# Kernel tuning notes

Hardware: AMD Instinct MI355X
Metric: run time of the kernel (lower is better)

## Reference

```python
import jax, jax.numpy as jnp
import numpy as np

IN, EMB, RNN, OUT = 2, 64, 128, 2
SEQ, PEDS, PRED = 20, 16384, 30


def setup_inputs() -> dict:
    key = jax.random.key(0)
    ks = jax.random.split(key, 6)
    def w(k, shape, fan_in):
        bound = 1.0 / np.sqrt(fan_in)
        return jax.random.uniform(k, shape, jnp.float32, -bound, bound)
    return {
        "observed_batch": jax.random.normal(ks[0], (SEQ, PEDS, IN), jnp.float32),
        "W_emb": w(ks[1], (EMB, IN), IN),
        "b_emb": jnp.zeros((EMB,), jnp.float32),
        "W_ih": w(ks[2], (4 * RNN, EMB), RNN),
        "b_ih": jnp.zeros((4 * RNN,), jnp.float32),
        "W_hh": w(ks[3], (4 * RNN, RNN), RNN),
        "b_hh": jnp.zeros((4 * RNN,), jnp.float32),
        "W_out": w(ks[4], (OUT, RNN), RNN),
        "b_out": jnp.zeros((OUT,), jnp.float32),
        "pred_len": PRED,
    }


def _lstm_cell(x, h, c, W_ih, b_ih, W_hh, b_hh):
    # torch.nn.LSTMCell gate order: i, f, g, o
    gates = x @ W_ih.T + b_ih + h @ W_hh.T + b_hh  # [peds, 4*RNN]
    i, f, g, o = jnp.split(gates, 4, axis=-1)
    i = jax.nn.sigmoid(i)
    f = jax.nn.sigmoid(f)
    g = jnp.tanh(g)
    o = jax.nn.sigmoid(o)
    c_new = f * c + i * g
    h_new = o * jnp.tanh(c_new)
    return h_new, c_new


def reference(observed_batch, W_emb, b_emb, W_ih, b_ih, W_hh, b_hh, W_out, b_out, pred_len):
    peds = observed_batch.shape[1]
    h0 = jnp.zeros((peds, RNN), observed_batch.dtype)
    c0 = jnp.zeros((peds, RNN), observed_batch.dtype)

    # Encode observed steps (dropout is identity in eval mode).
    def enc_step(carry, x_t):
        h, c = carry
        e = jax.nn.relu(x_t @ W_emb.T + b_emb)
        h, c = _lstm_cell(e, h, c, W_ih, b_ih, W_hh, b_hh)
        return (h, c), None

    (h, c), _ = jax.lax.scan(enc_step, (h0, c0), observed_batch)
    # Only the last step's output_layer result is consumed (faithful to source).
    out = h @ W_out.T + b_out  # [peds, OUT]

    def dec_step(carry, _):
        h, c, out = carry
        e = jax.nn.relu(out @ W_emb.T + b_emb)
        h, c = _lstm_cell(e, h, c, W_ih, b_ih, W_hh, b_hh)
        out = h @ W_out.T + b_out
        return (h, c, out), out

    _, output_seq = jax.lax.scan(dec_step, (h, c, out), None, length=pred_len)
    return jnp.squeeze(output_seq)  # [pred_len, peds, 2] (squeeze is a no-op here)
```

## Files before the change

### kernel.cpp

```cpp
#include <hip/hip_runtime.h>
#include <hip/hip_bf16.h>

#define SEQ   20
#define PRED  30
#define TSTEPS (SEQ + PRED)
#define PEDS  16384
#define EMB   64
#define RNN   128
#define PB    64
#define NT    512
#define L2E   1.44269504f

typedef _Float16 half8 __attribute__((ext_vector_type(8)));
typedef __attribute__((ext_vector_type(4))) float f32x4;
typedef __attribute__((ext_vector_type(2))) float f32x2;

#define RAW_BAR() do {                                          \
    asm volatile("s_waitcnt lgkmcnt(0)" ::: "memory");          \
    __builtin_amdgcn_s_barrier();                               \
    asm volatile("" ::: "memory");                              \
    __builtin_amdgcn_sched_barrier(0);                          \
} while (0)

__device__ __forceinline__ float sigm2(float xp) {
    return __builtin_amdgcn_rcpf(1.f + __builtin_amdgcn_exp2f(-xp));
}
__device__ __forceinline__ float tanh2p(float xp) {
    float r = __builtin_amdgcn_rcpf(__builtin_amdgcn_exp2f(xp + xp) + 1.f);
    return fmaf(-2.f, r, 1.f);
}
__device__ __forceinline__ float tanh2u(float x) {
    float r = __builtin_amdgcn_rcpf(__builtin_amdgcn_exp2f(x * (2.f * L2E)) + 1.f);
    return fmaf(-2.f, r, 1.f);
}

__global__ void prep_kernel(const float* __restrict__ Wih, const float* __restrict__ Whh,
                            const float* __restrict__ Wemb, const float* __restrict__ bemb,
                            _Float16* __restrict__ Bp, float* __restrict__ ewp) {
    int t = blockIdx.x * blockDim.x + threadIdx.x;
    if (t < 64) {
        ewp[t * 4 + 0] = Wemb[t * 2 + 0];
        ewp[t * 4 + 1] = Wemb[t * 2 + 1];
        ewp[t * 4 + 2] = bemb[t];
        ewp[t * 4 + 3] = 0.f;
    }
    if (t >= 6 * 32 * 64 * 8) return;
    int i  = t & 7;
    int l  = (t >> 3) & 63;
    int nt = (t >> 9) & 31;
    int kt = t >> 14;
    int n = (nt >> 3) * RNN + (nt & 7) * 16 + (l & 15);
    int k = kt * 32 + ((l >> 4) << 3) + i;
    float val = (k < EMB) ? Wih[n * EMB + k] : Whh[n * RNN + (k - EMB)];
    Bp[t] = (_Float16)(val * L2E);
}

__global__ __launch_bounds__(NT, 2) void lstm_kernel(
    const float* __restrict__ obs,
    const float* __restrict__ ewp,
    const float* __restrict__ bih,  const float* __restrict__ bhh,
    const _Float16* __restrict__ Bp,
    const float* __restrict__ Wout, const float* __restrict__ bout,
    float* __restrict__ out)
{
    __shared__ __align__(16) char smA[2 * 24576];
    __shared__ __align__(16) char smB[3 * 32768];
    __shared__ float smObs[SEQ * 128];
    __shared__ float smEW[64 * 4];
    __shared__ float smWO[256];
    __shared__ float part[64 * 2 * 4];
    __shared__ float outs[64 * 2];

    const int tid = threadIdx.x;
    const int l   = tid & 63;
    const int w   = __builtin_amdgcn_readfirstlane(tid >> 6);

    for (int r = tid; r < (2 * 24576) / 4; r += NT) ((int*)smA)[r] = 0;
    if (tid < 64) *(f32x4*)(smEW + tid * 4) = *(const f32x4*)(ewp + tid * 4);
    if (tid < 256) smWO[tid] = Wout[tid];
    for (int i = tid; i < SEQ * 128; i += NT) {
        int st = i >> 7, r = i & 127;
        smObs[i] = obs[(size_t)st * (PEDS * 2) + blockIdx.x * 128 + r];
    }

    const int jlane = w * 16 + (l & 15);
    const int lrow  = (l >> 4) << 2;
    const int swz   = (l & 7) << 4;

    float bias[4];
#pragma unroll
    for (int g = 0; g < 4; ++g) {
        int n = g * RNN + jlane;
        bias[g] = (bih[n] + bhh[n]) * L2E;
    }

    int aBase[4];
#pragma unroll
    for (int mt = 0; mt < 4; ++mt) {
        int ped = mt * 16 + (l & 15);
        aBase[mt] = ped * 384 + ((l >> 4) << 4);
    }
    int sAddr[4];
#pragma unroll
    for (int r = 0; r < 4; ++r) {
        int ped = lrow + r;
        sAddr[r] = (ped * 384 + 128 + jlane * 2) ^ ((ped & 7) << 4);
    }
    const int eAddr = (l * 384 + w * 16) ^ swz;
    const int oBase = l * 384 + 128 + (w >> 1) * 64;
    const char* bb  = smB + l * 16;
    const char* stageSrc = (const char*)Bp + l * 16 + w * 1024;
    const float* woBase = smWO + (w & 1) * 128 + (w >> 1) * 32;

    auto stage = [&](int slice) {
        const int buf = slice % 3;
#pragma unroll
        for (int g = 0; g < 4; ++g) {
            const void* src = stageSrc + slice * 32768 + g * 8192;
            __builtin_amdgcn_global_load_lds(
                (const __attribute__((address_space(1))) void*)src,
                (__attribute__((address_space(3))) void*)(smB + buf * 32768 + (g * 8 + w) * 1024),
                16, 0, 0);
        }
    };

    float c[16];
#pragma unroll
    for (int q = 0; q < 16; ++q) c[q] = 0.f;

    stage(0);
    stage(1);
    __syncthreads();

    int curOff = 0;

    for (int step = 0; step < TSTEPS; ++step) {
        const int nxtOff = curOff ^ 24576;

        {
            float x0, x1;
            if (step < SEQ) {
                f32x2 xv = *(const f32x2*)(smObs + step * 128 + l * 2);
                x0 = xv[0]; x1 = xv[1];
            } else {
                x0 = outs[l * 2 + 0];
                x1 = outs[l * 2 + 1];
            }
            half8 vh;
#pragma unroll
            for (int q = 0; q < 8; ++q) {
                const f32x4 ew = *(const f32x4*)(smEW + (w * 8 + q) * 4);
                float v = fmaf(x0, ew[0], fmaf(x1, ew[1], ew[2]));
                vh[q] = (_Float16)fmaxf(v, 0.f);
            }
            *(half8*)(smA + curOff + eAddr) = vh;
        }
        RAW_BAR();

        f32x4 acc[4][4];
#pragma unroll
        for (int mt = 0; mt < 4; ++mt)
#pragma unroll
            for (int g = 0; g < 4; ++g) {
                acc[mt][g][0] = bias[g]; acc[mt][g][1] = bias[g];
                acc[mt][g][2] = bias[g]; acc[mt][g][3] = bias[g];
            }
#pragma unroll
        for (int kt = 0; kt < 6; ++kt) {
            const int buf = kt % 3;
            stage((kt < 4) ? kt + 2 : kt - 4);
            asm volatile("s_waitcnt vmcnt(8)" ::: "memory");
            half8 bf[4];
#pragma unroll
            for (int g = 0; g < 4; ++g)
                bf[g] = *(const half8*)(bb + buf * 32768 + (g * 8 + w) * 1024);
#pragma unroll
            for (int mt = 0; mt < 4; ++mt) {
                half8 ah = *(const half8*)(smA + curOff + ((aBase[mt] + kt * 64) ^ swz));
#pragma unroll
                for (int g = 0; g < 4; ++g)
                    acc[mt][g] = __builtin_amdgcn_mfma_f32_16x16x32_f16(ah, bf[g], acc[mt][g], 0, 0, 0);
            }
        }

#pragma unroll
        for (int mt = 0; mt < 4; ++mt) {
#pragma unroll
            for (int r = 0; r < 4; ++r) {
                float gi = acc[mt][0][r], gf = acc[mt][1][r];
                float gg = acc[mt][2][r], go = acc[mt][3][r];
                float i_ = sigm2(gi), f_ = sigm2(gf), g_ = tanh2p(gg), o_ = sigm2(go);
                float cn = fmaf(f_, c[mt * 4 + r], i_ * g_);
                c[mt * 4 + r] = cn;
                float hn = o_ * tanh2u(cn);
                *(_Float16*)(smA + nxtOff + sAddr[r] + mt * 6144) = (_Float16)hn;
            }
        }

        if (step >= SEQ - 1) {
            RAW_BAR();
            {
                const int oo = w & 1;
                float s = 0.f;
#pragma unroll
                for (int t = 0; t < 4; ++t) {
                    half8 hh8 = *(const half8*)(smA + nxtOff + ((oBase + t * 16) ^ swz));
                    const f32x4 w0 = *(const f32x4*)(woBase + t * 8);
                    const f32x4 w1 = *(const f32x4*)(woBase + t * 8 + 4);
#pragma unroll
                    for (int i = 0; i < 4; ++i) {
                        s = fmaf((float)hh8[i], w0[i], s);
                        s = fmaf((float)hh8[i + 4], w1[i], s);
                    }
                }
                part[(l * 2 + oo) * 4 + (w >> 1)] = s;
            }
            RAW_BAR();
            if (tid < 128) {
                int pp = tid & 63, o2 = tid >> 6;
                const float* pr = &part[(pp * 2 + o2) * 4];
                float o = bout[o2] + ((pr[0] + pr[1]) + (pr[2] + pr[3]));
                outs[pp * 2 + o2] = o;
                if (step >= SEQ)
                    out[((size_t)(step - SEQ) * PEDS + blockIdx.x * PB + pp) * 2 + o2] = o;
            }
            RAW_BAR();
        }
        curOff = nxtOff;
    }
}

extern "C" void kernel_launch(void* const* d_in, const int* in_sizes, int n_in,
                              void* d_out, int out_size, void* d_ws, size_t ws_size,
                              hipStream_t stream) {
    const float* obs  = (const float*)d_in[0];
    const float* Wemb = (const float*)d_in[1];
    const float* bemb = (const float*)d_in[2];
    const float* Wih  = (const float*)d_in[3];
    const float* bih  = (const float*)d_in[4];
    const float* Whh  = (const float*)d_in[5];
    const float* bhh  = (const float*)d_in[6];
    const float* Wout = (const float*)d_in[7];
    const float* bout = (const float*)d_in[8];

    _Float16* Bp  = (_Float16*)d_ws;
    float*    ewp = (float*)(Bp + 6 * 32 * 64 * 8);

    prep_kernel<<<(6 * 32 * 64 * 8 + 255) / 256, 256, 0, stream>>>(Wih, Whh, Wemb, bemb, Bp, ewp);
    lstm_kernel<<<PEDS / PB, NT, 0, stream>>>(obs, ewp, bih, bhh, Bp, Wout, bout, (float*)d_out);
}
```

Baseline: 228.1 us.

## Fold output projection into decoder embedding via MFMA and double-buffer weight staging

Decoder steps no longer compute the output layer with scalar dot products, cross-wave partial sums and three barriers. Instead the prep kernel folds W_out into W_emb and b_emb, so the next embedding and the output come straight from h through a small fp16 MFMA over a 16x80 weight tile kept in LDS. The output is written one step late, with a final epilogue for the last step. Weight staging drops from triple to double buffering to make LDS room for the folded matrix, which may expose load latency, and fp16 rounding of the folded weights changes numerics slightly.

```diff
diff --git a/kernel.cpp b/kernel.cpp
--- a/kernel.cpp
+++ b/kernel.cpp
@@ -36,13 +36,25 @@
 
 __global__ void prep_kernel(const float* __restrict__ Wih, const float* __restrict__ Whh,
                             const float* __restrict__ Wemb, const float* __restrict__ bemb,
-                            _Float16* __restrict__ Bp, float* __restrict__ ewp) {
+                            const float* __restrict__ Wout, const float* __restrict__ bout,
+                            _Float16* __restrict__ Bp, float* __restrict__ ewp,
+                            _Float16* __restrict__ Xp, float* __restrict__ bfold) {
     int t = blockIdx.x * blockDim.x + threadIdx.x;
     if (t < 64) {
         ewp[t * 4 + 0] = Wemb[t * 2 + 0];
         ewp[t * 4 + 1] = Wemb[t * 2 + 1];
         ewp[t * 4 + 2] = bemb[t];
         ewp[t * 4 + 3] = 0.f;
+        bfold[t] = bemb[t] + Wemb[t * 2 + 0] * bout[0] + Wemb[t * 2 + 1] * bout[1];
+    }
+    if (t < 5 * 4 * 64 * 8) {
+        int i = t & 7, l = (t >> 3) & 63, ktp = (t >> 9) & 3, tile = t >> 11;
+        int c = tile * 16 + (l & 15);
+        int k = ktp * 32 + ((l >> 4) << 3) + i;
+        float v;
+        if (c < 64) v = Wemb[c * 2 + 0] * Wout[k] + Wemb[c * 2 + 1] * Wout[RNN + k];
+        else { int o = c - 64; v = (o < 2) ? Wout[o * RNN + k] : 0.f; }
+        Xp[t] = (_Float16)v;
     }
     if (t >= 6 * 32 * 64 * 8) return;
     int i  = t & 7;
@@ -59,25 +71,23 @@
     const float* __restrict__ obs,
     const float* __restrict__ ewp,
     const float* __restrict__ bih,  const float* __restrict__ bhh,
-    const _Float16* __restrict__ Bp,
-    const float* __restrict__ Wout, const float* __restrict__ bout,
+    const _Float16* __restrict__ Bp, const _Float16* __restrict__ Xp,
+    const float* __restrict__ bfold_g, const float* __restrict__ bout,
     float* __restrict__ out)
 {
     __shared__ __align__(16) char smA[2 * 24576];
-    __shared__ __align__(16) char smB[3 * 32768];
+    __shared__ __align__(16) char smB[2 * 32768];
+    __shared__ __align__(16) char smX[20480];
     __shared__ float smObs[SEQ * 128];
     __shared__ float smEW[64 * 4];
-    __shared__ float smWO[256];
-    __shared__ float part[64 * 2 * 4];
-    __shared__ float outs[64 * 2];
 
     const int tid = threadIdx.x;
     const int l   = tid & 63;
     const int w   = __builtin_amdgcn_readfirstlane(tid >> 6);
 
     for (int r = tid; r < (2 * 24576) / 4; r += NT) ((int*)smA)[r] = 0;
+    for (int r = tid; r < 20480 / 4; r += NT) ((int*)smX)[r] = ((const int*)Xp)[r];
     if (tid < 64) *(f32x4*)(smEW + tid * 4) = *(const f32x4*)(ewp + tid * 4);
-    if (tid < 256) smWO[tid] = Wout[tid];
     for (int i = tid; i < SEQ * 128; i += NT) {
         int st = i >> 7, r = i & 127;
         smObs[i] = obs[(size_t)st * (PEDS * 2) + blockIdx.x * 128 + r];
@@ -94,12 +104,25 @@
         bias[g] = (bih[n] + bhh[n]) * L2E;
     }
 
+    const int nU = (w < 4) ? 3 : 2;
+    int uT[3], uM[3];
+#pragma unroll
+    for (int j = 0; j < 3; ++j) { int u = w + j * 8; uT[j] = u % 5; uM[j] = u / 5; }
+    const float bo2 = ((l & 15) < 2) ? bout[l & 15] : 0.f;
+    float bx[3];
+    int axA[3], xAd[3], exCol2[3];
+    const int aB0 = (l & 15) * 384 + ((l >> 4) << 4);
+#pragma unroll
+    for (int j = 0; j < 3; ++j) {
+        bx[j]     = (uT[j] < 4) ? bfold_g[uT[j] * 16 + (l & 15)] : bo2;
+        axA[j]    = aB0 + uM[j] * 6144;
+        xAd[j]    = uT[j] * 4096 + l * 16;
+        exCol2[j] = (uT[j] * 16 + (l & 15)) * 2;
+    }
+
     int aBase[4];
 #pragma unroll
-    for (int mt = 0; mt < 4; ++mt) {
-        int ped = mt * 16 + (l & 15);
-        aBase[mt] = ped * 384 + ((l >> 4) << 4);
-    }
+    for (int mt = 0; mt < 4; ++mt) aBase[mt] = aB0 + mt * 6144;
     int sAddr[4];
 #pragma unroll
     for (int r = 0; r < 4; ++r) {
@@ -107,16 +130,13 @@
         sAddr[r] = (ped * 384 + 128 + jlane * 2) ^ ((ped & 7) << 4);
     }
     const int eAddr = (l * 384 + w * 16) ^ swz;
-    const int oBase = l * 384 + 128 + (w >> 1) * 64;
     const char* bb  = smB + l * 16;
     const char* stageSrc = (const char*)Bp + l * 16 + w * 1024;
-    const float* woBase = smWO + (w & 1) * 128 + (w >> 1) * 32;
-
-    auto stage = [&](int slice) {
-        const int buf = slice % 3;
+
+    auto stage = [&](int kt, int buf) {
 #pragma unroll
         for (int g = 0; g < 4; ++g) {
-            const void* src = stageSrc + slice * 32768 + g * 8192;
+            const void* src = stageSrc + kt * 32768 + g * 8192;
             __builtin_amdgcn_global_load_lds(
                 (const __attribute__((address_space(1))) void*)src,
                 (__attribute__((address_space(3))) void*)(smB + buf * 32768 + (g * 8 + w) * 1024),
@@ -128,8 +148,7 @@
 #pragma unroll
     for (int q = 0; q < 16; ++q) c[q] = 0.f;
 
-    stage(0);
-    stage(1);
+    stage(0, 0);
     __syncthreads();
 
     int curOff = 0;
@@ -137,25 +156,56 @@
     for (int step = 0; step < TSTEPS; ++step) {
         const int nxtOff = curOff ^ 24576;
 
-        {
-            float x0, x1;
-            if (step < SEQ) {
-                f32x2 xv = *(const f32x2*)(smObs + step * 128 + l * 2);
-                x0 = xv[0]; x1 = xv[1];
-            } else {
-                x0 = outs[l * 2 + 0];
-                x1 = outs[l * 2 + 1];
-            }
+        if (step < SEQ) {
+            f32x2 xv = *(const f32x2*)(smObs + step * 128 + l * 2);
             half8 vh;
 #pragma unroll
             for (int q = 0; q < 8; ++q) {
                 const f32x4 ew = *(const f32x4*)(smEW + (w * 8 + q) * 4);
-                float v = fmaf(x0, ew[0], fmaf(x1, ew[1], ew[2]));
+                float v = fmaf(xv[0], ew[0], fmaf(xv[1], ew[1], ew[2]));
                 vh[q] = (_Float16)fmaxf(v, 0.f);
             }
             *(half8*)(smA + curOff + eAddr) = vh;
-        }
-        RAW_BAR();
+            RAW_BAR();
+        } else {
+            RAW_BAR();
+            f32x4 ax[3];
+#pragma unroll
+            for (int j = 0; j < 3; ++j) {
+                ax[j][0] = bx[j]; ax[j][1] = bx[j]; ax[j][2] = bx[j]; ax[j][3] = bx[j];
+            }
+#pragma unroll
+            for (int ktp = 0; ktp < 4; ++ktp) {
+#pragma unroll
+                for (int j = 0; j < 3; ++j) {
+                    if (j < nU) {
+                        half8 ah = *(const half8*)(smA + curOff + ((axA[j] + (ktp + 2) * 64) ^ swz));
+                        half8 xb = *(const half8*)(smX + xAd[j] + ktp * 1024);
+                        ax[j] = __builtin_amdgcn_mfma_f32_16x16x32_f16(ah, xb, ax[j], 0, 0, 0);
+                    }
+                }
+            }
+#pragma unroll
+            for (int j = 0; j < 3; ++j) {
+                if (j < nU) {
+                    if (uT[j] < 4) {
+#pragma unroll
+                        for (int r = 0; r < 4; ++r) {
+                            int ped = uM[j] * 16 + lrow + r;
+                            int off = (ped * 384 + exCol2[j]) ^ ((ped & 7) << 4);
+                            *(_Float16*)(smA + curOff + off) = (_Float16)fmaxf(ax[j][r], 0.f);
+                        }
+                    } else if ((l & 15) < 2 && step > SEQ) {
+#pragma unroll
+                        for (int r = 0; r < 4; ++r) {
+                            int ped = uM[j] * 16 + lrow + r;
+                            out[((size_t)(step - 1 - SEQ) * PEDS + blockIdx.x * PB + ped) * 2 + (l & 15)] = ax[j][r];
+                        }
+                    }
+                }
+            }
+            RAW_BAR();
+        }
 
         f32x4 acc[4][4];
 #pragma unroll
@@ -167,9 +217,10 @@
             }
 #pragma unroll
         for (int kt = 0; kt < 6; ++kt) {
-            const int buf = kt % 3;
-            stage((kt < 4) ? kt + 2 : kt - 4);
-            asm volatile("s_waitcnt vmcnt(8)" ::: "memory");
+            const int buf = kt & 1;
+            const int ktn = (kt < 5) ? kt + 1 : 0;
+            stage(ktn, buf ^ 1);
+            asm volatile("s_waitcnt vmcnt(4)" ::: "memory");
             half8 bf[4];
 #pragma unroll
             for (int g = 0; g < 4; ++g)
@@ -196,37 +247,29 @@
                 *(_Float16*)(smA + nxtOff + sAddr[r] + mt * 6144) = (_Float16)hn;
             }
         }
-
-        if (step >= SEQ - 1) {
-            RAW_BAR();
-            {
-                const int oo = w & 1;
-                float s = 0.f;
-#pragma unroll
-                for (int t = 0; t < 4; ++t) {
-                    half8 hh8 = *(const half8*)(smA + nxtOff + ((oBase + t * 16) ^ swz));
-                    const f32x4 w0 = *(const f32x4*)(woBase + t * 8);
-                    const f32x4 w1 = *(const f32x4*)(woBase + t * 8 + 4);
-#pragma unroll
-                    for (int i = 0; i < 4; ++i) {
-                        s = fmaf((float)hh8[i], w0[i], s);
-                        s = fmaf((float)hh8[i + 4], w1[i], s);
-                    }
+        curOff = nxtOff;
+    }
+
+    RAW_BAR();
+#pragma unroll
+    for (int j = 0; j < 3; ++j) {
+        if (j < nU && uT[j] == 4) {
+            f32x4 ax;
+            ax[0] = bx[j]; ax[1] = bx[j]; ax[2] = bx[j]; ax[3] = bx[j];
+#pragma unroll
+            for (int ktp = 0; ktp < 4; ++ktp) {
+                half8 ah = *(const half8*)(smA + curOff + ((axA[j] + (ktp + 2) * 64) ^ swz));
+                half8 xb = *(const half8*)(smX + xAd[j] + ktp * 1024);
+                ax = __builtin_amdgcn_mfma_f32_16x16x32_f16(ah, xb, ax, 0, 0, 0);
+            }
+            if ((l & 15) < 2) {
+#pragma unroll
+                for (int r = 0; r < 4; ++r) {
+                    int ped = uM[j] * 16 + lrow + r;
+                    out[((size_t)(PRED - 1) * PEDS + blockIdx.x * PB + ped) * 2 + (l & 15)] = ax[r];
                 }
-                part[(l * 2 + oo) * 4 + (w >> 1)] = s;
-            }
-            RAW_BAR();
-            if (tid < 128) {
-                int pp = tid & 63, o2 = tid >> 6;
-                const float* pr = &part[(pp * 2 + o2) * 4];
-                float o = bout[o2] + ((pr[0] + pr[1]) + (pr[2] + pr[3]));
-                outs[pp * 2 + o2] = o;
-                if (step >= SEQ)
-                    out[((size_t)(step - SEQ) * PEDS + blockIdx.x * PB + pp) * 2 + o2] = o;
-            }
-            RAW_BAR();
-        }
-        curOff = nxtOff;
+            }
+        }
     }
 }
 
@@ -243,9 +286,12 @@
     const float* Wout = (const float*)d_in[7];
     const float* bout = (const float*)d_in[8];
 
-    _Float16* Bp  = (_Float16*)d_ws;
-    float*    ewp = (float*)(Bp + 6 * 32 * 64 * 8);
-
-    prep_kernel<<<(6 * 32 * 64 * 8 + 255) / 256, 256, 0, stream>>>(Wih, Whh, Wemb, bemb, Bp, ewp);
-    lstm_kernel<<<PEDS / PB, NT, 0, stream>>>(obs, ewp, bih, bhh, Bp, Wout, bout, (float*)d_out);
-}
+    _Float16* Bp    = (_Float16*)d_ws;
+    float*    ewp   = (float*)(Bp + 6 * 32 * 64 * 8);
+    _Float16* Xp    = (_Float16*)(ewp + 256);
+    float*    bfold = (float*)(Xp + 10240);
+
+    prep_kernel<<<(6 * 32 * 64 * 8 + 255) / 256, 256, 0, stream>>>(
+        Wih, Whh, Wemb, bemb, Wout, bout, Bp, ewp, Xp, bfold);
+    lstm_kernel<<<PEDS / PB, NT, 0, stream>>>(obs, ewp, bih, bhh, Bp, Xp, bfold, bout, (float*)d_out);
+}
```

New measurement: 268.6 us. 1.18x slower.
